# Kernel tuning notes

Measured on AMD Instinct MI355X. Metric: run time of the kernel, lower is better.

## Reference

```python
import jax, jax.numpy as jnp
import numpy as np

B, T, H, E = 256, 256, 512, 96  # batch, enc seq len, hidden/enc dim, charset size


def setup_inputs() -> dict:
    key = jax.random.key(0)
    ks = jax.random.split(key, 9)
    s = 0.05  # param scale
    return {
        "prev_h": jax.random.normal(ks[0], (B, H), jnp.float32),
        "prev_c": jax.random.normal(ks[1], (B, H), jnp.float32),
        "batch_H": jax.random.normal(ks[2], (B, T, H), jnp.float32),
        "char_onehots": jax.nn.one_hot(jax.random.randint(ks[3], (B,), 0, E), E, dtype=jnp.float32),
        "W_i2h": jax.random.normal(ks[4], (H, H), jnp.float32) * s,
        "W_h2h": jax.random.normal(ks[5], (H, H), jnp.float32) * s,
        "b_h2h": jnp.zeros((H,), jnp.float32),
        "w_score": jax.random.normal(ks[6], (H, 1), jnp.float32) * s,
        "W_lstm": jax.random.normal(ks[7], (H + E, 4 * H), jnp.float32) * s,
        "U_lstm": jax.random.normal(ks[8], (H, 4 * H), jnp.float32) * s,
        "b_lstm": jnp.zeros((4 * H,), jnp.float32),
    }


def reference(prev_h, prev_c, batch_H, char_onehots,
              W_i2h, W_h2h, b_h2h, w_score, W_lstm, U_lstm, b_lstm):
    # Additive (Bahdanau) attention
    proj = jnp.einsum('btd,dh->bth', batch_H, W_i2h)          # [B,T,H]
    hp = prev_h @ W_h2h + b_h2h                               # [B,H]
    e = jnp.tanh(proj + hp[:, None, :]) @ w_score             # [B,T,1]
    alpha = jax.nn.softmax(e, axis=1)                         # [B,T,1]
    context = jnp.einsum('bt,btd->bd', alpha[..., 0], batch_H)  # [B,D]
    x = jnp.concatenate([context, char_onehots], axis=1)      # [B,D+E]
    # Keras LSTMCell: gate order i, f, c(g), o
    z = x @ W_lstm + prev_h @ U_lstm + b_lstm                 # [B,4H]
    i, f, g, o = jnp.split(z, 4, axis=1)
    c_new = jax.nn.sigmoid(f) * prev_c + jax.nn.sigmoid(i) * jnp.tanh(g)
    h_new = jax.nn.sigmoid(o) * jnp.tanh(c_new)
    return h_new, c_new, alpha
```

## Files before the change

kernel.cpp:

```cpp
#include <hip/hip_runtime.h>
#include <hip/hip_bf16.h>
#include <math.h>

#define Bq 256
#define Tq 256
#define Hq 512
#define Eq 96

typedef __attribute__((ext_vector_type(8))) short short8;
typedef __attribute__((ext_vector_type(4))) float f32x4;

static __device__ __forceinline__ unsigned short f2bf(float f) {
  union { float f; unsigned u; } v; v.f = f;
  unsigned r = v.u + 0x7FFF + ((v.u >> 16) & 1);
  return (unsigned short)(r >> 16);
}

static __device__ __forceinline__ float sat_tanh(float x) {
  float ax = fminf(fabsf(x), 15.0f);
  float e = __builtin_exp2f(ax * 2.885390082f);
  float t = 1.0f - 2.0f / (e + 1.0f);
  return copysignf(t, x);
}

static __device__ __forceinline__ float sat_sig(float x) {
  float cx = fmaxf(fminf(x, 30.0f), -30.0f);
  return 1.0f / (1.0f + __builtin_exp2f(-cx * 1.442695041f));
}

__global__ __launch_bounds__(256) void convW_k(const float* __restrict__ W,
                                               unsigned short* __restrict__ Wt) {
  __shared__ float tile[32][33];
  int bx = blockIdx.x & 15, by = blockIdx.x >> 4;
  int tx = threadIdx.x & 31, ty = threadIdx.x >> 5;
  #pragma unroll
  for (int i = 0; i < 32; i += 8)
    tile[ty + i][tx] = W[(size_t)(by * 32 + ty + i) * Hq + bx * 32 + tx];
  __syncthreads();
  #pragma unroll
  for (int i = 0; i < 32; i += 8)
    Wt[(size_t)(bx * 32 + ty + i) * Hq + by * 32 + tx] = f2bf(tile[tx][ty + i]);
}

__global__ __launch_bounds__(256) void hsplit_k(const float* __restrict__ ph,
                                                const float* __restrict__ Whh,
                                                float* __restrict__ hp) {
  __shared__ __align__(16) float xs[8][128];
  const int ks = blockIdx.x & 3;
  const int nc = (blockIdx.x >> 2) & 3;
  const int bg = blockIdx.x >> 4;
  const int tid = threadIdx.x;
  const int row0 = bg * 8;
  const int d0 = ks * 128;
  for (int i = tid; i < 8 * 32; i += 256) {
    int r = i >> 5, dd = (i & 31) * 4;
    *(float4*)&xs[r][dd] = *(const float4*)&ph[(size_t)(row0 + r) * Hq + d0 + dd];
  }
  __syncthreads();
  const int rt = tid >> 6;
  const int ct = tid & 63;
  const int n = nc * 128 + ct * 2;
  float a00 = 0, a01 = 0, a10 = 0, a11 = 0;
  for (int dd = 0; dd < 128; dd += 4) {
    float4 x0 = *(const float4*)&xs[rt * 2][dd];
    float4 x1 = *(const float4*)&xs[rt * 2 + 1][dd];
    #pragma unroll
    for (int j = 0; j < 4; j++) {
      float2 w = *(const float2*)&Whh[(size_t)(d0 + dd + j) * Hq + n];
      float xj0 = ((const float*)&x0)[j];
      float xj1 = ((const float*)&x1)[j];
      a00 += xj0 * w.x; a01 += xj0 * w.y;
      a10 += xj1 * w.x; a11 += xj1 * w.y;
    }
  }
  int row = row0 + rt * 2;
  atomicAdd(&hp[(size_t)row * Hq + n], a00);
  atomicAdd(&hp[(size_t)row * Hq + n + 1], a01);
  atomicAdd(&hp[(size_t)(row + 1) * Hq + n], a10);
  atomicAdd(&hp[(size_t)(row + 1) * Hq + n + 1], a11);
}

#define BM 128
#define BN 128
#define BK 32
#define LDK 40

__global__ __launch_bounds__(256) void fused_score_k(
    const float* __restrict__ A,
    const unsigned short* __restrict__ Wt,
    const float* __restrict__ hp,
    const float* __restrict__ bh,
    const float* __restrict__ wsc,
    float* __restrict__ e) {
  __shared__ unsigned short As[BM * LDK];
  __shared__ unsigned short Bs[BN * LDK];
  __shared__ float hps[BN];
  __shared__ float wss[BN];

  const int tid = threadIdx.x;
  const int m0 = blockIdx.x * BM;
  const int n0 = blockIdx.y * BN;
  const int bb = m0 >> 8;

  if (tid < BN) {
    hps[tid] = hp[(size_t)bb * Hq + n0 + tid] + bh[n0 + tid];
    wss[tid] = wsc[n0 + tid];
  }

  const int wave = tid >> 6;
  const int lane = tid & 63;
  const int quad = lane >> 4;
  const int l16 = lane & 15;
  const int wm = (wave & 1) * 64;
  const int wn = (wave >> 1) * 64;

  f32x4 acc[4][4] = {};

  const int arow = tid >> 3;
  const int acol = (tid & 7) * 4;
  const int brow = tid >> 2;
  const int bkh = (tid & 3) * 8;

  for (int k0 = 0; k0 < Hq; k0 += BK) {
    __syncthreads();
    #pragma unroll
    for (int p = 0; p < 4; p++) {
      int r = arow + p * 32;
      const float4 v = *(const float4*)(&A[(size_t)(m0 + r) * Hq + k0 + acol]);
      ushort4 pk;
      pk.x = f2bf(v.x); pk.y = f2bf(v.y); pk.z = f2bf(v.z); pk.w = f2bf(v.w);
      *(ushort4*)&As[r * LDK + acol] = pk;
    }
    #pragma unroll
    for (int p = 0; p < 2; p++) {
      int r = brow + p * 64;
      const uint4 v = *(const uint4*)(&Wt[(size_t)(n0 + r) * Hq + k0 + bkh]);
      *(uint4*)&Bs[r * LDK + bkh] = v;
    }
    __syncthreads();

    short8 af[4], bfr[4];
    #pragma unroll
    for (int mi = 0; mi < 4; mi++)
      af[mi] = *(const short8*)&As[(wm + mi * 16 + l16) * LDK + quad * 8];
    #pragma unroll
    for (int ni = 0; ni < 4; ni++)
      bfr[ni] = *(const short8*)&Bs[(wn + ni * 16 + l16) * LDK + quad * 8];
    #pragma unroll
    for (int mi = 0; mi < 4; mi++)
      #pragma unroll
      for (int ni = 0; ni < 4; ni++)
        acc[mi][ni] = __builtin_amdgcn_mfma_f32_16x16x32_bf16(
            af[mi], bfr[ni], acc[mi][ni], 0, 0, 0);
  }

  float hv[4], wv[4];
  #pragma unroll
  for (int ni = 0; ni < 4; ni++) {
    int c = wn + ni * 16 + l16;
    hv[ni] = hps[c];
    wv[ni] = wss[c];
  }
  #pragma unroll
  for (int mi = 0; mi < 4; mi++) {
    float s[4] = {0, 0, 0, 0};
    #pragma unroll
    for (int ni = 0; ni < 4; ni++)
      #pragma unroll
      for (int r = 0; r < 4; r++)
        s[r] += sat_tanh(acc[mi][ni][r] + hv[ni]) * wv[ni];
    #pragma unroll
    for (int r = 0; r < 4; r++) {
      s[r] += __shfl_xor(s[r], 8, 64);
      s[r] += __shfl_xor(s[r], 4, 64);
      s[r] += __shfl_xor(s[r], 2, 64);
      s[r] += __shfl_xor(s[r], 1, 64);
    }
    if (l16 == 0) {
      int row = m0 + wm + mi * 16 + quad * 4;
      #pragma unroll
      for (int r = 0; r < 4; r++) atomicAdd(&e[row + r], s[r]);
    }
  }
}

__global__ __launch_bounds__(256) void softmax_k(float* __restrict__ ea) {
  __shared__ float red[8];
  int b = blockIdx.x, t = threadIdx.x;
  int wave = t >> 6, lane = t & 63;
  float x = ea[b * Tq + t];
  float m = x;
  #pragma unroll
  for (int off = 32; off >= 1; off >>= 1) m = fmaxf(m, __shfl_xor(m, off, 64));
  if (lane == 0) red[wave] = m;
  __syncthreads();
  m = fmaxf(fmaxf(red[0], red[1]), fmaxf(red[2], red[3]));
  float ex = __builtin_exp2f((x - m) * 1.442695041f);
  float s = ex;
  #pragma unroll
  for (int off = 32; off >= 1; off >>= 1) s += __shfl_xor(s, off, 64);
  if (lane == 0) red[4 + wave] = s;
  __syncthreads();
  s = red[4] + red[5] + red[6] + red[7];
  ea[b * Tq + t] = ex / s;
}

__global__ __launch_bounds__(256) void ctxsplit_k(const float* __restrict__ alpha,
                                                  const float* __restrict__ bH,
                                                  float* __restrict__ ctx) {
  __shared__ float al[64];
  const int b = blockIdx.x >> 2;
  const int tc = blockIdx.x & 3;
  const int tid = threadIdx.x;
  if (tid < 64) al[tid] = alpha[b * Tq + tc * 64 + tid];
  __syncthreads();
  const float2* Hp = (const float2*)(bH + (size_t)b * Tq * Hq + (size_t)tc * 64 * Hq);
  float ax = 0.f, ay = 0.f;
  #pragma unroll 8
  for (int t = 0; t < 64; t++) {
    float a = al[t];
    float2 v = Hp[t * (Hq / 2) + tid];
    ax += a * v.x;
    ay += a * v.y;
  }
  atomicAdd(&ctx[(size_t)b * Hq + 2 * tid], ax);
  atomicAdd(&ctx[(size_t)b * Hq + 2 * tid + 1], ay);
}

__global__ __launch_bounds__(256) void zsplit_k(
    const float* __restrict__ ctx, const float* __restrict__ oneh,
    const float* __restrict__ ph, const float* __restrict__ Wl,
    const float* __restrict__ Ul, float* __restrict__ z) {
  __shared__ __align__(16) float xs[8 * 280];
  const int ks = blockIdx.x & 3;
  const int hc = (blockIdx.x >> 2) & 7;
  const int bg = blockIdx.x >> 5;
  const int tid = threadIdx.x;
  const int row0 = bg * 8;
  const int dbase = ks * 280;

  for (int i = tid; i < 8 * 280; i += 256) {
    int r = i / 280, dd = i % 280;
    int g = dbase + dd;
    float v;
    if (g < 512) v = ctx[(size_t)(row0 + r) * Hq + g];
    else if (g < 608) v = oneh[(row0 + r) * Eq + (g - 512)];
    else v = ph[(size_t)(row0 + r) * Hq + (g - 608)];
    xs[r * 280 + dd] = v;
  }
  __syncthreads();

  const int rt = tid >> 6;
  const int ct = tid & 63;
  const int c0 = ct * 4;
  const int gate = c0 >> 6;
  const int ho = c0 & 63;
  const int n = gate * 512 + hc * 64 + ho;

  float acc0[4] = {0, 0, 0, 0};
  float acc1[4] = {0, 0, 0, 0};
  const float* xr0 = &xs[(rt * 2) * 280];
  const float* xr1 = &xs[(rt * 2 + 1) * 280];

  for (int dd = 0; dd < 280; dd += 4) {
    float4 x0 = *(const float4*)&xr0[dd];
    float4 x1 = *(const float4*)&xr1[dd];
    #pragma unroll
    for (int j = 0; j < 4; j++) {
      int d = dbase + dd + j;
      const float* wp = (d < 608) ? &Wl[(size_t)d * 2048 + n]
                                  : &Ul[(size_t)(d - 608) * 2048 + n];
      float4 w = *(const float4*)wp;
      float a = ((const float*)&x0)[j], b = ((const float*)&x1)[j];
      acc0[0] += a * w.x; acc0[1] += a * w.y; acc0[2] += a * w.z; acc0[3] += a * w.w;
      acc1[0] += b * w.x; acc1[1] += b * w.y; acc1[2] += b * w.z; acc1[3] += b * w.w;
    }
  }
  const int r0 = row0 + rt * 2;
  #pragma unroll
  for (int j = 0; j < 4; j++) {
    atomicAdd(&z[(size_t)r0 * 2048 + n + j], acc0[j]);
    atomicAdd(&z[(size_t)(r0 + 1) * 2048 + n + j], acc1[j]);
  }
}

__global__ __launch_bounds__(256) void gatesz_k(const float* __restrict__ z,
                                                const float* __restrict__ bl,
                                                const float* __restrict__ pc,
                                                float* __restrict__ outh,
                                                float* __restrict__ outc) {
  int p = blockIdx.x * 256 + threadIdx.x;
  #pragma unroll
  for (int q = 0; q < 2; q++, p += 65536) {
    int r = p >> 9, h = p & 511;
    const float* zb = z + (size_t)r * 2048;
    float gi = zb[h] + bl[h];
    float gf = zb[512 + h] + bl[512 + h];
    float gg = zb[1024 + h] + bl[1024 + h];
    float go = zb[1536 + h] + bl[1536 + h];
    float cn = sat_sig(gf) * pc[p] + sat_sig(gi) * sat_tanh(gg);
    float hn = sat_sig(go) * sat_tanh(cn);
    outh[p] = hn;
    outc[p] = cn;
  }
}

#define KXc 1120
__global__ __launch_bounds__(256) void zgates2_k(
    const float* __restrict__ ctx, const float* __restrict__ oneh,
    const float* __restrict__ ph, const float* __restrict__ pc,
    const float* __restrict__ Wl, const float* __restrict__ Ul,
    const float* __restrict__ bl,
    float* __restrict__ outh, float* __restrict__ outc) {
  __shared__ __align__(16) float xs[8 * KXc];
  const int bg = blockIdx.x >> 3;
  const int hc = blockIdx.x & 7;
  const int tid = threadIdx.x;
  const int row0 = bg * 8;

  for (int i = tid; i < 8 * 128; i += 256) {
    int r = i >> 7, dd = (i & 127) * 4;
    *(float4*)&xs[r * KXc + dd] = *(const float4*)&ctx[(size_t)(row0 + r) * Hq + dd];
  }
  for (int i = tid; i < 8 * 128; i += 256) {
    int r = i >> 7, dd = (i & 127) * 4;
    *(float4*)&xs[r * KXc + 608 + dd] = *(const float4*)&ph[(size_t)(row0 + r) * Hq + dd];
  }
  if (tid < 8 * 24) {
    int r = tid / 24, dd = (tid % 24) * 4;
    *(float4*)&xs[r * KXc + 512 + dd] = *(const float4*)&oneh[(row0 + r) * Eq + dd];
  }
  __syncthreads();

  const int rt = tid >> 6;
  const int ct = tid & 63;
  const int c0 = ct * 4;
  const int gate = c0 >> 6;
  const int ho = c0 & 63;
  const int n = gate * 512 + hc * 64 + ho;

  float acc0[4] = {0, 0, 0, 0};
  float acc1[4] = {0, 0, 0, 0};
  const float* xr0 = &xs[(rt * 2) * KXc];
  const float* xr1 = &xs[(rt * 2 + 1) * KXc];

  for (int d = 0; d < 608; d += 4) {
    float4 x0 = *(const float4*)&xr0[d];
    float4 x1 = *(const float4*)&xr1[d];
    #pragma unroll
    for (int j = 0; j < 4; j++) {
      float4 w = *(const float4*)&Wl[(size_t)(d + j) * 2048 + n];
      float a = ((const float*)&x0)[j], b = ((const float*)&x1)[j];
      acc0[0] += a * w.x; acc0[1] += a * w.y; acc0[2] += a * w.z; acc0[3] += a * w.w;
      acc1[0] += b * w.x; acc1[1] += b * w.y; acc1[2] += b * w.z; acc1[3] += b * w.w;
    }
  }
  for (int d = 0; d < 512; d += 4) {
    float4 x0 = *(const float4*)&xr0[608 + d];
    float4 x1 = *(const float4*)&xr1[608 + d];
    #pragma unroll
    for (int j = 0; j < 4; j++) {
      float4 w = *(const float4*)&Ul[(size_t)(d + j) * 2048 + n];
      float a = ((const float*)&x0)[j], b = ((const float*)&x1)[j];
      acc0[0] += a * w.x; acc0[1] += a * w.y; acc0[2] += a * w.z; acc0[3] += a * w.w;
      acc1[0] += b * w.x; acc1[1] += b * w.y; acc1[2] += b * w.z; acc1[3] += b * w.w;
    }
  }

  __syncthreads();
  float* zs = xs;
  #pragma unroll
  for (int j = 0; j < 4; j++) {
    zs[(rt * 2) * 256 + c0 + j] = acc0[j];
    zs[(rt * 2 + 1) * 256 + c0 + j] = acc1[j];
  }
  __syncthreads();

  #pragma unroll
  for (int p = tid; p < 512; p += 256) {
    int r = p >> 6, o = p & 63;
    int h = hc * 64 + o;
    int grow = row0 + r;
    float gi = zs[r * 256 + o]       + bl[h];
    float gf = zs[r * 256 + 64 + o]  + bl[512 + h];
    float gg = zs[r * 256 + 128 + o] + bl[1024 + h];
    float go = zs[r * 256 + 192 + o] + bl[1536 + h];
    float cn = sat_sig(gf) * pc[(size_t)grow * Hq + h] + sat_sig(gi) * sat_tanh(gg);
    float hn = sat_sig(go) * sat_tanh(cn);
    outh[(size_t)grow * Hq + h] = hn;
    outc[(size_t)grow * Hq + h] = cn;
  }
}

extern "C" void kernel_launch(void* const* d_in, const int* in_sizes, int n_in,
                              void* d_out, int out_size, void* d_ws, size_t ws_size,
                              hipStream_t stream) {
  const float* prev_h = (const float*)d_in[0];
  const float* prev_c = (const float*)d_in[1];
  const float* batch_H = (const float*)d_in[2];
  const float* oneh = (const float*)d_in[3];
  const float* W_i2h = (const float*)d_in[4];
  const float* W_h2h = (const float*)d_in[5];
  const float* b_h2h = (const float*)d_in[6];
  const float* w_score = (const float*)d_in[7];
  const float* W_lstm = (const float*)d_in[8];
  const float* U_lstm = (const float*)d_in[9];
  const float* b_lstm = (const float*)d_in[10];

  float* out = (float*)d_out;
  float* outh = out;
  float* outc = out + Bq * Hq;
  float* alpha = out + 2 * Bq * Hq;

  float* ws = (float*)d_ws;
  float* hp = ws;
  float* ctx = ws;
  unsigned short* Wt = (unsigned short*)(ws + 131072);
  float* z = ws + 131072;

  const bool bigws = ws_size >= 2621440;

  hipMemsetAsync(alpha, 0, Bq * Tq * sizeof(float), stream);
  hipMemsetAsync(hp, 0, Bq * Hq * sizeof(float), stream);
  convW_k<<<256, 256, 0, stream>>>(W_i2h, Wt);
  hsplit_k<<<512, 256, 0, stream>>>(prev_h, W_h2h, hp);
  dim3 g2(512, 4);
  fused_score_k<<<g2, 256, 0, stream>>>(batch_H, Wt, hp, b_h2h, w_score, alpha);
  softmax_k<<<256, 256, 0, stream>>>(alpha);
  if (bigws) {
    hipMemsetAsync(ws, 0, 2621440, stream);
    ctxsplit_k<<<1024, 256, 0, stream>>>(alpha, batch_H, ctx);
    zsplit_k<<<1024, 256, 0, stream>>>(ctx, oneh, prev_h, W_lstm, U_lstm, z);
    gatesz_k<<<256, 256, 0, stream>>>(z, b_lstm, prev_c, outh, outc);
  } else {
    hipMemsetAsync(ctx, 0, Bq * Hq * sizeof(float), stream);
    ctxsplit_k<<<1024, 256, 0, stream>>>(alpha, batch_H, ctx);
    zgates2_k<<<256, 256, 0, stream>>>(ctx, oneh, prev_h, prev_c,
                                       W_lstm, U_lstm, b_lstm, outh, outc);
  }
}
```

Measured before the change: 399.1 us.

## Restructure attention score GEMM so each block covers full N and reads A once

The score kernel now handles 64 rows with the full 512-wide hidden dimension in each block. It converts the whole A tile to bf16 in LDS once, and each wave streams its 128 columns of the bf16 weight from global memory in registers, prefetching the next K step. This removes the 4x re-reading and re-conversion of batch_H across the N-blocks and the per-K-step barriers. Because each block produces complete row scores, the atomic adds and the memset of the score buffer go away. The tradeoffs are a large LDS footprint (about 66KB) and more accumulator registers, which lower occupancy, and every block fetches the full weight matrix from L2.

After: 455.0 us. 1.14x slower.

```diff
diff --git a/kernel.cpp b/kernel.cpp
--- a/kernel.cpp
+++ b/kernel.cpp
@@ -80,84 +80,86 @@
   atomicAdd(&hp[(size_t)(row + 1) * Hq + n + 1], a11);
 }
 
-#define BM 128
-#define BN 128
-#define BK 32
-#define LDK 40
-
-__global__ __launch_bounds__(256) void fused_score_k(
+#define SBM 64
+#define LDA 520
+
+__global__ __launch_bounds__(256) void score2_k(
     const float* __restrict__ A,
     const unsigned short* __restrict__ Wt,
     const float* __restrict__ hp,
     const float* __restrict__ bh,
     const float* __restrict__ wsc,
     float* __restrict__ e) {
-  __shared__ unsigned short As[BM * LDK];
-  __shared__ unsigned short Bs[BN * LDK];
-  __shared__ float hps[BN];
-  __shared__ float wss[BN];
+  __shared__ unsigned short As[SBM * LDA];
+  __shared__ float hps[Hq];
+  __shared__ float wss[Hq];
+  __shared__ float eps[4][SBM];
 
   const int tid = threadIdx.x;
-  const int m0 = blockIdx.x * BM;
-  const int n0 = blockIdx.y * BN;
+  const int m0 = blockIdx.x * SBM;
   const int bb = m0 >> 8;
 
-  if (tid < BN) {
-    hps[tid] = hp[(size_t)bb * Hq + n0 + tid] + bh[n0 + tid];
-    wss[tid] = wsc[n0 + tid];
-  }
+  #pragma unroll
+  for (int i = tid; i < Hq; i += 256) {
+    hps[i] = hp[(size_t)bb * Hq + i] + bh[i];
+    wss[i] = wsc[i];
+  }
+  #pragma unroll
+  for (int i = 0; i < 32; i++) {
+    int g = i * 256 + tid;
+    int r = g >> 7, c = (g & 127) * 4;
+    const float4 v = *(const float4*)&A[(size_t)(m0 + r) * Hq + c];
+    __hip_bfloat162 p0 = __float22bfloat162_rn({v.x, v.y});
+    __hip_bfloat162 p1 = __float22bfloat162_rn({v.z, v.w});
+    ushort4 pk;
+    pk.x = *(unsigned short*)&p0.x; pk.y = *(unsigned short*)&p0.y;
+    pk.z = *(unsigned short*)&p1.x; pk.w = *(unsigned short*)&p1.y;
+    *(ushort4*)&As[r * LDA + c] = pk;
+  }
+  __syncthreads();
 
   const int wave = tid >> 6;
   const int lane = tid & 63;
   const int quad = lane >> 4;
   const int l16 = lane & 15;
-  const int wm = (wave & 1) * 64;
-  const int wn = (wave >> 1) * 64;
-
-  f32x4 acc[4][4] = {};
-
-  const int arow = tid >> 3;
-  const int acol = (tid & 7) * 4;
-  const int brow = tid >> 2;
-  const int bkh = (tid & 3) * 8;
-
-  for (int k0 = 0; k0 < Hq; k0 += BK) {
-    __syncthreads();
-    #pragma unroll
-    for (int p = 0; p < 4; p++) {
-      int r = arow + p * 32;
-      const float4 v = *(const float4*)(&A[(size_t)(m0 + r) * Hq + k0 + acol]);
-      ushort4 pk;
-      pk.x = f2bf(v.x); pk.y = f2bf(v.y); pk.z = f2bf(v.z); pk.w = f2bf(v.w);
-      *(ushort4*)&As[r * LDK + acol] = pk;
-    }
-    #pragma unroll
-    for (int p = 0; p < 2; p++) {
-      int r = brow + p * 64;
-      const uint4 v = *(const uint4*)(&Wt[(size_t)(n0 + r) * Hq + k0 + bkh]);
-      *(uint4*)&Bs[r * LDK + bkh] = v;
-    }
-    __syncthreads();
-
-    short8 af[4], bfr[4];
+  const int nw = wave * 128;
+
+  f32x4 acc[4][8] = {};
+
+  const unsigned short* bp[8];
+  #pragma unroll
+  for (int ni = 0; ni < 8; ni++)
+    bp[ni] = &Wt[(size_t)(nw + ni * 16 + l16) * Hq + quad * 8];
+
+  short8 bc[8];
+  #pragma unroll
+  for (int ni = 0; ni < 8; ni++) bc[ni] = *(const short8*)bp[ni];
+
+  for (int k0 = 0; k0 < Hq; k0 += 32) {
+    short8 bn[8];
+    if (k0 + 32 < Hq) {
+      #pragma unroll
+      for (int ni = 0; ni < 8; ni++)
+        bn[ni] = *(const short8*)(bp[ni] + k0 + 32);
+    }
+    short8 af[4];
     #pragma unroll
     for (int mi = 0; mi < 4; mi++)
-      af[mi] = *(const short8*)&As[(wm + mi * 16 + l16) * LDK + quad * 8];
-    #pragma unroll
-    for (int ni = 0; ni < 4; ni++)
-      bfr[ni] = *(const short8*)&Bs[(wn + ni * 16 + l16) * LDK + quad * 8];
+      af[mi] = *(const short8*)&As[(mi * 16 + l16) * LDA + k0 + quad * 8];
     #pragma unroll
     for (int mi = 0; mi < 4; mi++)
       #pragma unroll
-      for (int ni = 0; ni < 4; ni++)
+      for (int ni = 0; ni < 8; ni++)
         acc[mi][ni] = __builtin_amdgcn_mfma_f32_16x16x32_bf16(
-            af[mi], bfr[ni], acc[mi][ni], 0, 0, 0);
-  }
-
-  float hv[4], wv[4];
-  #pragma unroll
-  for (int ni = 0; ni < 4; ni++) {
-    int c = wn + ni * 16 + l16;
+            af[mi], bc[ni], acc[mi][ni], 0, 0, 0);
+    #pragma unroll
+    for (int ni = 0; ni < 8; ni++) bc[ni] = bn[ni];
+  }
+
+  float hv[8], wv[8];
+  #pragma unroll
+  for (int ni = 0; ni < 8; ni++) {
+    int c = nw + ni * 16 + l16;
     hv[ni] = hps[c];
     wv[ni] = wss[c];
   }
@@ -165,7 +167,7 @@
   for (int mi = 0; mi < 4; mi++) {
     float s[4] = {0, 0, 0, 0};
     #pragma unroll
-    for (int ni = 0; ni < 4; ni++)
+    for (int ni = 0; ni < 8; ni++)
       #pragma unroll
       for (int r = 0; r < 4; r++)
         s[r] += sat_tanh(acc[mi][ni][r] + hv[ni]) * wv[ni];
@@ -177,11 +179,13 @@
       s[r] += __shfl_xor(s[r], 1, 64);
     }
     if (l16 == 0) {
-      int row = m0 + wm + mi * 16 + quad * 4;
       #pragma unroll
-      for (int r = 0; r < 4; r++) atomicAdd(&e[row + r], s[r]);
-    }
-  }
+      for (int r = 0; r < 4; r++) eps[wave][mi * 16 + quad * 4 + r] = s[r];
+    }
+  }
+  __syncthreads();
+  if (tid < SBM)
+    e[m0 + tid] = eps[0][tid] + eps[1][tid] + eps[2][tid] + eps[3][tid];
 }
 
 __global__ __launch_bounds__(256) void softmax_k(float* __restrict__ ea) {
@@ -420,12 +424,10 @@
 
   const bool bigws = ws_size >= 2621440;
 
-  hipMemsetAsync(alpha, 0, Bq * Tq * sizeof(float), stream);
   hipMemsetAsync(hp, 0, Bq * Hq * sizeof(float), stream);
   convW_k<<<256, 256, 0, stream>>>(W_i2h, Wt);
   hsplit_k<<<512, 256, 0, stream>>>(prev_h, W_h2h, hp);
-  dim3 g2(512, 4);
-  fused_score_k<<<g2, 256, 0, stream>>>(batch_H, Wt, hp, b_h2h, w_score, alpha);
+  score2_k<<<1024, 256, 0, stream>>>(batch_H, Wt, hp, b_h2h, w_score, alpha);
   softmax_k<<<256, 256, 0, stream>>>(alpha);
   if (bigws) {
     hipMemsetAsync(ws, 0, 2621440, stream);
```

## Pre-convert batch_H to bf16 once and reuse it for score and context

Applied to the files above, without the earlier changes.

When the workspace is large enough, a new pass converts batch_H to bf16 into the workspace. The score GEMM then loads bf16 tiles directly, and the context reduction also reads the bf16 copy, halving its read traffic. The score grid is flattened to 1D with the n-tile as the fast index so the four n-tiles sharing an A tile run close together. This adds a full extra pass over batch_H (read fp32, write bf16), and context is now computed from bf16-rounded values. Whether the new path runs depends on the harness giving a workspace of about 70MB.

Result: slower. 411.0 us (+3.0%).

```diff
diff --git a/kernel.cpp b/kernel.cpp
--- a/kernel.cpp
+++ b/kernel.cpp
@@ -14,6 +14,10 @@
   union { float f; unsigned u; } v; v.f = f;
   unsigned r = v.u + 0x7FFF + ((v.u >> 16) & 1);
   return (unsigned short)(r >> 16);
+}
+static __device__ __forceinline__ float bf2f(unsigned short s) {
+  union { unsigned u; float f; } v; v.u = ((unsigned)s) << 16;
+  return v.f;
 }
 
 static __device__ __forceinline__ float sat_tanh(float x) {
@@ -40,6 +44,18 @@
   #pragma unroll
   for (int i = 0; i < 32; i += 8)
     Wt[(size_t)(bx * 32 + ty + i) * Hq + by * 32 + tx] = f2bf(tile[tx][ty + i]);
+}
+
+__global__ __launch_bounds__(256) void convA_k(const float* __restrict__ A,
+                                               unsigned short* __restrict__ Ab) {
+  size_t g = (size_t)blockIdx.x * 256 + threadIdx.x;
+  #pragma unroll
+  for (int i = 0; i < 16; i++, g += 524288) {
+    const float4 v = ((const float4*)A)[g];
+    ushort4 pk;
+    pk.x = f2bf(v.x); pk.y = f2bf(v.y); pk.z = f2bf(v.z); pk.w = f2bf(v.w);
+    ((ushort4*)Ab)[g] = pk;
+  }
 }
 
 __global__ __launch_bounds__(256) void hsplit_k(const float* __restrict__ ph,
@@ -85,21 +101,20 @@
 #define BK 32
 #define LDK 40
 
-__global__ __launch_bounds__(256) void fused_score_k(
-    const float* __restrict__ A,
+__global__ __launch_bounds__(256) void score_bf_k(
+    const unsigned short* __restrict__ Ab,
     const unsigned short* __restrict__ Wt,
-    const float* __restrict__ hp,
-    const float* __restrict__ bh,
-    const float* __restrict__ wsc,
-    float* __restrict__ e) {
+    const float* __restrict__ hp, const float* __restrict__ bh,
+    const float* __restrict__ wsc, float* __restrict__ e) {
   __shared__ unsigned short As[BM * LDK];
   __shared__ unsigned short Bs[BN * LDK];
   __shared__ float hps[BN];
   __shared__ float wss[BN];
 
   const int tid = threadIdx.x;
-  const int m0 = blockIdx.x * BM;
-  const int n0 = blockIdx.y * BN;
+  const int gid = blockIdx.x;
+  const int m0 = (gid >> 2) * BM;
+  const int n0 = (gid & 3) * BN;
   const int bb = m0 >> 8;
 
   if (tid < BN) {
@@ -116,6 +131,96 @@
 
   f32x4 acc[4][4] = {};
 
+  const int srow = tid >> 2;
+  const int scol = (tid & 3) * 8;
+
+  for (int k0 = 0; k0 < Hq; k0 += BK) {
+    __syncthreads();
+    #pragma unroll
+    for (int p = 0; p < 2; p++) {
+      int r = srow + p * 64;
+      *(uint4*)&As[r * LDK + scol] =
+          *(const uint4*)&Ab[(size_t)(m0 + r) * Hq + k0 + scol];
+      *(uint4*)&Bs[r * LDK + scol] =
+          *(const uint4*)&Wt[(size_t)(n0 + r) * Hq + k0 + scol];
+    }
+    __syncthreads();
+
+    short8 af[4], bfr[4];
+    #pragma unroll
+    for (int mi = 0; mi < 4; mi++)
+      af[mi] = *(const short8*)&As[(wm + mi * 16 + l16) * LDK + quad * 8];
+    #pragma unroll
+    for (int ni = 0; ni < 4; ni++)
+      bfr[ni] = *(const short8*)&Bs[(wn + ni * 16 + l16) * LDK + quad * 8];
+    #pragma unroll
+    for (int mi = 0; mi < 4; mi++)
+      #pragma unroll
+      for (int ni = 0; ni < 4; ni++)
+        acc[mi][ni] = __builtin_amdgcn_mfma_f32_16x16x32_bf16(
+            af[mi], bfr[ni], acc[mi][ni], 0, 0, 0);
+  }
+
+  float hv[4], wv[4];
+  #pragma unroll
+  for (int ni = 0; ni < 4; ni++) {
+    int c = wn + ni * 16 + l16;
+    hv[ni] = hps[c];
+    wv[ni] = wss[c];
+  }
+  #pragma unroll
+  for (int mi = 0; mi < 4; mi++) {
+    float s[4] = {0, 0, 0, 0};
+    #pragma unroll
+    for (int ni = 0; ni < 4; ni++)
+      #pragma unroll
+      for (int r = 0; r < 4; r++)
+        s[r] += sat_tanh(acc[mi][ni][r] + hv[ni]) * wv[ni];
+    #pragma unroll
+    for (int r = 0; r < 4; r++) {
+      s[r] += __shfl_xor(s[r], 8, 64);
+      s[r] += __shfl_xor(s[r], 4, 64);
+      s[r] += __shfl_xor(s[r], 2, 64);
+      s[r] += __shfl_xor(s[r], 1, 64);
+    }
+    if (l16 == 0) {
+      int row = m0 + wm + mi * 16 + quad * 4;
+      #pragma unroll
+      for (int r = 0; r < 4; r++) atomicAdd(&e[row + r], s[r]);
+    }
+  }
+}
+
+__global__ __launch_bounds__(256) void score_f32_k(
+    const float* __restrict__ A,
+    const unsigned short* __restrict__ Wt,
+    const float* __restrict__ hp, const float* __restrict__ bh,
+    const float* __restrict__ wsc, float* __restrict__ e) {
+  __shared__ unsigned short As[BM * LDK];
+  __shared__ unsigned short Bs[BN * LDK];
+  __shared__ float hps[BN];
+  __shared__ float wss[BN];
+
+  const int tid = threadIdx.x;
+  const int gid = blockIdx.x;
+  const int m0 = (gid >> 2) * BM;
+  const int n0 = (gid & 3) * BN;
+  const int bb = m0 >> 8;
+
+  if (tid < BN) {
+    hps[tid] = hp[(size_t)bb * Hq + n0 + tid] + bh[n0 + tid];
+    wss[tid] = wsc[n0 + tid];
+  }
+
+  const int wave = tid >> 6;
+  const int lane = tid & 63;
+  const int quad = lane >> 4;
+  const int l16 = lane & 15;
+  const int wm = (wave & 1) * 64;
+  const int wn = (wave >> 1) * 64;
+
+  f32x4 acc[4][4] = {};
+
   const int arow = tid >> 3;
   const int acol = (tid & 7) * 4;
   const int brow = tid >> 2;
@@ -203,6 +308,28 @@
   __syncthreads();
   s = red[4] + red[5] + red[6] + red[7];
   ea[b * Tq + t] = ex / s;
+}
+
+__global__ __launch_bounds__(256) void ctxb_k(const float* __restrict__ alpha,
+                                              const unsigned short* __restrict__ Ab,
+                                              float* __restrict__ ctx) {
+  __shared__ float al[64];
+  const int b = blockIdx.x >> 2;
+  const int tc = blockIdx.x & 3;
+  const int tid = threadIdx.x;
+  if (tid < 64) al[tid] = alpha[b * Tq + tc * 64 + tid];
+  __syncthreads();
+  const unsigned short* Hp = Ab + (size_t)b * Tq * Hq + (size_t)tc * 64 * Hq;
+  float ax = 0.f, ay = 0.f;
+  #pragma unroll 8
+  for (int t = 0; t < 64; t++) {
+    float a = al[t];
+    unsigned v = *(const unsigned*)&Hp[t * Hq + 2 * tid];
+    ax += a * bf2f((unsigned short)(v & 0xFFFF));
+    ay += a * bf2f((unsigned short)(v >> 16));
+  }
+  atomicAdd(&ctx[(size_t)b * Hq + 2 * tid], ax);
+  atomicAdd(&ctx[(size_t)b * Hq + 2 * tid + 1], ay);
 }
 
 __global__ __launch_bounds__(256) void ctxsplit_k(const float* __restrict__ alpha,
@@ -416,23 +543,37 @@
   float* hp = ws;
   float* ctx = ws;
   unsigned short* Wt = (unsigned short*)(ws + 131072);
-  float* z = ws + 131072;
-
+
+  const bool hugews = ws_size >= 70254592;
   const bool bigws = ws_size >= 2621440;
 
   hipMemsetAsync(alpha, 0, Bq * Tq * sizeof(float), stream);
   hipMemsetAsync(hp, 0, Bq * Hq * sizeof(float), stream);
   convW_k<<<256, 256, 0, stream>>>(W_i2h, Wt);
   hsplit_k<<<512, 256, 0, stream>>>(prev_h, W_h2h, hp);
-  dim3 g2(512, 4);
-  fused_score_k<<<g2, 256, 0, stream>>>(batch_H, Wt, hp, b_h2h, w_score, alpha);
-  softmax_k<<<256, 256, 0, stream>>>(alpha);
-  if (bigws) {
+
+  if (hugews) {
+    unsigned short* Ab = (unsigned short*)(ws + 262144);
+    float* z = ws + 17039360;
+    convA_k<<<2048, 256, 0, stream>>>(batch_H, Ab);
+    score_bf_k<<<2048, 256, 0, stream>>>(Ab, Wt, hp, b_h2h, w_score, alpha);
+    softmax_k<<<256, 256, 0, stream>>>(alpha);
+    hipMemsetAsync(ctx, 0, Bq * Hq * sizeof(float), stream);
+    hipMemsetAsync(z, 0, Bq * 2048 * sizeof(float), stream);
+    ctxb_k<<<1024, 256, 0, stream>>>(alpha, Ab, ctx);
+    zsplit_k<<<1024, 256, 0, stream>>>(ctx, oneh, prev_h, W_lstm, U_lstm, z);
+    gatesz_k<<<256, 256, 0, stream>>>(z, b_lstm, prev_c, outh, outc);
+  } else if (bigws) {
+    float* z = ws + 131072;
+    score_f32_k<<<2048, 256, 0, stream>>>(batch_H, Wt, hp, b_h2h, w_score, alpha);
+    softmax_k<<<256, 256, 0, stream>>>(alpha);
     hipMemsetAsync(ws, 0, 2621440, stream);
     ctxsplit_k<<<1024, 256, 0, stream>>>(alpha, batch_H, ctx);
     zsplit_k<<<1024, 256, 0, stream>>>(ctx, oneh, prev_h, W_lstm, U_lstm, z);
     gatesz_k<<<256, 256, 0, stream>>>(z, b_lstm, prev_c, outh, outc);
   } else {
+    score_f32_k<<<2048, 256, 0, stream>>>(batch_H, Wt, hp, b_h2h, w_score, alpha);
+    softmax_k<<<256, 256, 0, stream>>>(alpha);
     hipMemsetAsync(ctx, 0, Bq * Hq * sizeof(float), stream);
     ctxsplit_k<<<1024, 256, 0, stream>>>(alpha, batch_H, ctx);
     zgates2_k<<<256, 256, 0, stream>>>(ctx, oneh, prev_h, prev_c,
```
